# Kernel tuning notes

Hardware: AMD Instinct MI355X
Metric: run time of the kernel (lower is better)

The kernel has to match this reference:

```python
import jax, jax.numpy as jnp
import numpy as np

H = 2880      # hidden_size
I = 2880      # intermediate_size
E = 8         # num_experts
K = 4         # experts_per_token
N = 1024      # num tokens
EPS = 1e-5
ALPHA = 1.702
BETA = 1.0


def setup_inputs() -> dict:
    key = jax.random.key(0)
    ks = jax.random.split(key, 8)
    s = 0.02
    return {
        "x": jax.random.normal(ks[0], (N, H), jnp.float32),
        "norm_w": jnp.ones((H,), jnp.float32),
        "gate_w": jax.random.normal(ks[1], (E, H), jnp.float32) * s,
        "gate_b": jax.random.normal(ks[2], (E,), jnp.float32) * s,
        "w_gate_up": jax.random.normal(ks[3], (E, 2 * I, H), jnp.float32) * s,
        "b_gate_up": jax.random.normal(ks[4], (E, 2 * I), jnp.float32) * s,
        "w_down": jax.random.normal(ks[5], (E, H, I), jnp.float32) * s,
        "b_down": jax.random.normal(ks[6], (E, H), jnp.float32) * s,
    }


def reference(x, norm_w, gate_w, gate_b, w_gate_up, b_gate_up, w_down, b_down):
    # RMSNorm
    t = x * jax.lax.rsqrt(jnp.mean(x * x, axis=-1, keepdims=True) + EPS) * norm_w
    # Router gate (Linear with bias)
    logits = t @ gate_w.T + gate_b                      # [N, E]
    # Renormalize routing: top-k of logits, softmax over selected logits
    top_vals, top_idx = jax.lax.top_k(logits, K)        # [N, K]
    route_w = jax.nn.softmax(top_vals, axis=-1)         # [N, K]
    # Dense combine matrix [N, E] (zero for unselected experts)
    n_ar = jnp.arange(N)[:, None]
    R = jnp.zeros((N, E), t.dtype).at[n_ar, top_idx].add(route_w)
    # Fused gate_up projection per expert: [E, N, 2I]
    h = jnp.einsum('nh,eih->eni', t, w_gate_up) + b_gate_up[:, None, :]
    x_glu, x_lin = h[..., :I], h[..., I:]
    # SwiGLU with per-expert alpha/beta (all 1.702 / 1.0)
    act = x_glu * jax.nn.sigmoid(ALPHA * x_glu) * (x_lin + BETA)   # [E, N, I]
    # Down projection per expert: [E, N, H]
    outs = jnp.einsum('eni,ehi->enh', act, w_down) + b_down[:, None, :]
    # Weighted combine over selected experts + residual
    y = jnp.einsum('ne,enh->nh', R, outs)
    return x + y
```

## Files before the change

kernel.cpp:

```cpp
#include <hip/hip_runtime.h>
#include <hip/hip_bf16.h>

#define NTOK 1024
#define HDIM 2880
#define IDIM 2880
#define NEXP 8
#define BK 64
#define NT 45

typedef __attribute__((ext_vector_type(4))) float fx4;
typedef __attribute__((ext_vector_type(8))) short sx8;
typedef __attribute__((ext_vector_type(8))) unsigned short usx8;

typedef const __attribute__((address_space(1))) void* gas_p;
typedef __attribute__((address_space(3))) void* las_p;

__device__ __forceinline__ unsigned short f2bf(float f) {
  __hip_bfloat16 b = __float2bfloat16(f);
  return __builtin_bit_cast(unsigned short, b);
}
__device__ __forceinline__ usx8 cvt8(fx4 a, fx4 b) {
  usx8 u = {f2bf(a.x), f2bf(a.y), f2bf(a.z), f2bf(a.w),
            f2bf(b.x), f2bf(b.y), f2bf(b.z), f2bf(b.w)};
  return u;
}

#define MFMA16(a, b, c) __builtin_amdgcn_mfma_f32_16x16x32_bf16(a, b, c, 0, 0, 0)

__global__ __launch_bounds__(256) void init_out_k(const float* __restrict__ x,
                                                  float* __restrict__ out) {
  int i = blockIdx.x * 256 + threadIdx.x;
  ((fx4*)out)[i] = ((const fx4*)x)[i];
}

__global__ __launch_bounds__(256) void rms_router_k(
    const float* __restrict__ x, const float* __restrict__ norm_w,
    const float* __restrict__ gate_w, const float* __restrict__ gate_b,
    unsigned short* __restrict__ t_bf, int* __restrict__ cnt,
    int* __restrict__ tok, float* __restrict__ wgt) {
  const int n = blockIdx.x;
  const int tid = threadIdx.x;
  const int wid = tid >> 6, lane = tid & 63;
  const float* xr = x + (size_t)n * HDIM;

  float ss = 0.f;
  for (int h = tid; h < HDIM; h += 256) { float v = xr[h]; ss += v * v; }
  #pragma unroll
  for (int o = 32; o > 0; o >>= 1) ss += __shfl_down(ss, o);
  __shared__ float sred[4];
  if (lane == 0) sred[wid] = ss;
  __syncthreads();
  const float rstd =
      rsqrtf((sred[0] + sred[1] + sred[2] + sred[3]) * (1.0f / HDIM) + 1e-5f);

  float p[NEXP];
  #pragma unroll
  for (int e = 0; e < NEXP; e++) p[e] = 0.f;
  for (int h = tid; h < HDIM; h += 256) {
    float xv = xr[h] * norm_w[h];
    t_bf[(size_t)n * HDIM + h] = f2bf(xv * rstd);
    #pragma unroll
    for (int e = 0; e < NEXP; e++) p[e] += xv * gate_w[e * HDIM + h];
  }
  __shared__ float pls[4][NEXP];
  #pragma unroll
  for (int e = 0; e < NEXP; e++) {
    float v = p[e];
    #pragma unroll
    for (int o = 32; o > 0; o >>= 1) v += __shfl_down(v, o);
    if (lane == 0) pls[wid][e] = v;
  }
  __syncthreads();
  if (tid == 0) {
    float lg[NEXP];
    #pragma unroll
    for (int e = 0; e < NEXP; e++)
      lg[e] = (pls[0][e] + pls[1][e] + pls[2][e] + pls[3][e]) * rstd + gate_b[e];
    unsigned used = 0;
    float val[4];
    int idx[4];
    for (int k = 0; k < 4; k++) {
      float best = -1e30f;
      int bi = 0;
      for (int e = 0; e < NEXP; e++)
        if (!((used >> e) & 1u) && lg[e] > best) { best = lg[e]; bi = e; }
      used |= 1u << bi;
      val[k] = best;
      idx[k] = bi;
    }
    float sum = 0.f, w[4];
    for (int k = 0; k < 4; k++) { w[k] = expf(val[k] - val[0]); sum += w[k]; }
    for (int k = 0; k < 4; k++) {
      int e = idx[k];
      int slot = atomicAdd(&cnt[e], 1);
      tok[e * NTOK + slot] = n;
      wgt[e * NTOK + slot] = w[k] / sum;
    }
  }
}

__global__ __launch_bounds__(512, 4) void gemm1_k(
    const unsigned short* __restrict__ t_bf,
    const float* __restrict__ w_gate_up, const float* __restrict__ b_gate_up,
    const int* __restrict__ cnt, const int* __restrict__ tok,
    unsigned short* __restrict__ act_bf) {
  const int h = blockIdx.x;
  const int u = h >> 2, z = h & 3;
  const int e = u / 45;
  const int c0 = (u % 45) * 64;
  const int m0 = z * 256;
  const int ce = cnt[e];
  if (m0 >= ce) return;

  const int tid = threadIdx.x, lane = tid & 63, wid = tid >> 6;
  const int fr = lane & 15, fq = lane >> 4;
  const int wm = wid >> 1, wn = wid & 1;

  __shared__ __align__(16) unsigned short Ash[256 * 64];
  __shared__ __align__(16) unsigned short Bsh[128 * 64];

  const fx4 FZ = {0.f, 0.f, 0.f, 0.f};
  fx4 accG[4][2], accL[4][2];
  #pragma unroll
  for (int m = 0; m < 4; m++)
    #pragma unroll
    for (int n = 0; n < 2; n++) { accG[m][n] = FZ; accL[m][n] = FZ; }

  const unsigned short* gA[4];
  #pragma unroll
  for (int j = 0; j < 4; ++j) {
    int R = m0 + wid * 32 + j * 8 + (lane >> 3);
    int rc = R < ce ? R : ce - 1;
    gA[j] = t_bf + (size_t)tok[e * NTOK + rc] * HDIM +
            ((lane & 7) ^ ((lane >> 3) & 7)) * 8;
  }
  const int bR = tid >> 3, bC = tid & 7;
  const float* srcG = w_gate_up + (size_t)e * (2 * IDIM) * HDIM +
                      (size_t)(c0 + bR) * HDIM + bC * 8;
  const float* srcL = srcG + (size_t)IDIM * HDIM;
  const int bsw = (bC ^ (bR & 7)) * 8;

  fx4 rG0, rG1, rL0, rL1;
  rG0 = *(const fx4*)(srcG);
  rG1 = *(const fx4*)(srcG + 4);
  rL0 = *(const fx4*)(srcL);
  rL1 = *(const fx4*)(srcL + 4);

  for (int t = 0; t < NT; ++t) {
    const int ko = t * BK;
    __syncthreads();
    #pragma unroll
    for (int j = 0; j < 4; ++j)
      __builtin_amdgcn_global_load_lds((gas_p)(gA[j] + ko),
                                       (las_p)&Ash[(wid * 32 + j * 8) * 64], 16,
                                       0, 0);
    *(usx8*)&Bsh[bR * 64 + bsw] = cvt8(rG0, rG1);
    *(usx8*)&Bsh[(64 + bR) * 64 + bsw] = cvt8(rL0, rL1);
    __syncthreads();
    const int kf = (t + 1 < NT ? (t + 1) * BK : 0);
    rG0 = *(const fx4*)(srcG + kf);
    rG1 = *(const fx4*)(srcG + kf + 4);
    rL0 = *(const fx4*)(srcL + kf);
    rL1 = *(const fx4*)(srcL + kf + 4);
    #pragma unroll
    for (int ks = 0; ks < 2; ++ks) {
      const int rc = ks * 4 + fq;
      sx8 aF[4], bG[2], bL[2];
      #pragma unroll
      for (int m = 0; m < 4; ++m)
        aF[m] = *(const sx8*)&Ash[(wm * 64 + m * 16 + fr) * 64 +
                                  ((rc ^ (fr & 7)) * 8)];
      #pragma unroll
      for (int n = 0; n < 2; ++n) {
        bG[n] = *(const sx8*)&Bsh[(wn * 32 + n * 16 + fr) * 64 +
                                  ((rc ^ (fr & 7)) * 8)];
        bL[n] = *(const sx8*)&Bsh[(64 + wn * 32 + n * 16 + fr) * 64 +
                                  ((rc ^ (fr & 7)) * 8)];
      }
      __builtin_amdgcn_s_setprio(1);
      #pragma unroll
      for (int n = 0; n < 2; ++n)
        #pragma unroll
        for (int m = 0; m < 4; ++m) {
          accG[m][n] = MFMA16(aF[m], bG[n], accG[m][n]);
          accL[m][n] = MFMA16(aF[m], bL[n], accL[m][n]);
        }
      __builtin_amdgcn_s_setprio(0);
    }
  }

  #pragma unroll
  for (int n = 0; n < 2; ++n) {
    const int col = c0 + wn * 32 + n * 16 + fr;
    const float bg = b_gate_up[e * (2 * IDIM) + col];
    const float bl = b_gate_up[e * (2 * IDIM) + IDIM + col];
    #pragma unroll
    for (int m = 0; m < 4; ++m) {
      #pragma unroll
      for (int r = 0; r < 4; ++r) {
        int slot = m0 + wm * 64 + m * 16 + fq * 4 + r;
        if (slot < ce) {
          float g = accG[m][n][r] + bg;
          float l = accL[m][n][r] + bl;
          float a = g * (1.0f / (1.0f + __expf(-1.702f * g))) * (l + 1.0f);
          act_bf[((size_t)e * NTOK + slot) * IDIM + col] = f2bf(a);
        }
      }
    }
  }
}

__global__ __launch_bounds__(512, 4) void gemm2_k(
    const unsigned short* __restrict__ act_bf, const float* __restrict__ w_down,
    const float* __restrict__ b_down, const int* __restrict__ cnt,
    const int* __restrict__ tok, const float* __restrict__ wgt,
    float* __restrict__ out) {
  const int h = blockIdx.x;
  const int u = h >> 2, z = h & 3;
  const int e = u / 30;
  const int c0 = (u % 30) * 96;
  const int m0 = z * 256;
  const int ce = cnt[e];
  if (m0 >= ce) return;

  const int tid = threadIdx.x, lane = tid & 63, wid = tid >> 6;
  const int fr = lane & 15, fq = lane >> 4;
  const int wm = wid >> 1, wn = wid & 1;

  __shared__ __align__(16) unsigned short Ash[256 * 64];
  __shared__ __align__(16) unsigned short Bsh[96 * 64];

  const fx4 FZ = {0.f, 0.f, 0.f, 0.f};
  fx4 acc[4][3];
  #pragma unroll
  for (int m = 0; m < 4; m++)
    #pragma unroll
    for (int n = 0; n < 3; n++) acc[m][n] = FZ;

  const unsigned short* gA[4];
  #pragma unroll
  for (int j = 0; j < 4; ++j) {
    int R = m0 + wid * 32 + j * 8 + (lane >> 3);
    int rc = R < ce ? R : ce - 1;
    gA[j] = act_bf + ((size_t)e * NTOK + rc) * IDIM +
            ((lane & 7) ^ ((lane >> 3) & 7)) * 8;
  }
  const int bR0 = tid >> 3, bC0 = tid & 7;
  const float* wb = w_down + (size_t)e * HDIM * IDIM;
  const float* srcB0 = wb + (size_t)(c0 + bR0) * IDIM + bC0 * 8;
  const float* srcB1 = wb + (size_t)(c0 + 64 + bR0) * IDIM + bC0 * 8;
  const int bsw0 = (bC0 ^ (bR0 & 7)) * 8;

  fx4 r0a, r0b, r1a, r1b;
  r0a = *(const fx4*)(srcB0);
  r0b = *(const fx4*)(srcB0 + 4);
  if (tid < 256) {
    r1a = *(const fx4*)(srcB1);
    r1b = *(const fx4*)(srcB1 + 4);
  }

  for (int t = 0; t < NT; ++t) {
    const int ko = t * BK;
    __syncthreads();
    #pragma unroll
    for (int j = 0; j < 4; ++j)
      __builtin_amdgcn_global_load_lds((gas_p)(gA[j] + ko),
                                       (las_p)&Ash[(wid * 32 + j * 8) * 64], 16,
                                       0, 0);
    *(usx8*)&Bsh[bR0 * 64 + bsw0] = cvt8(r0a, r0b);
    if (tid < 256) *(usx8*)&Bsh[(64 + bR0) * 64 + bsw0] = cvt8(r1a, r1b);
    __syncthreads();
    const int kf = (t + 1 < NT ? (t + 1) * BK : 0);
    r0a = *(const fx4*)(srcB0 + kf);
    r0b = *(const fx4*)(srcB0 + kf + 4);
    if (tid < 256) {
      r1a = *(const fx4*)(srcB1 + kf);
      r1b = *(const fx4*)(srcB1 + kf + 4);
    }
    #pragma unroll
    for (int ks = 0; ks < 2; ++ks) {
      const int rc = ks * 4 + fq;
      sx8 aF[4], bB[3];
      #pragma unroll
      for (int m = 0; m < 4; ++m)
        aF[m] = *(const sx8*)&Ash[(wm * 64 + m * 16 + fr) * 64 +
                                  ((rc ^ (fr & 7)) * 8)];
      #pragma unroll
      for (int n = 0; n < 3; ++n)
        bB[n] = *(const sx8*)&Bsh[(wn * 48 + n * 16 + fr) * 64 +
                                  ((rc ^ (fr & 7)) * 8)];
      __builtin_amdgcn_s_setprio(1);
      #pragma unroll
      for (int n = 0; n < 3; ++n)
        #pragma unroll
        for (int m = 0; m < 4; ++m)
          acc[m][n] = MFMA16(aF[m], bB[n], acc[m][n]);
      __builtin_amdgcn_s_setprio(0);
    }
  }

  #pragma unroll
  for (int n = 0; n < 3; ++n) {
    const int col = c0 + wn * 48 + n * 16 + fr;
    const float bias = b_down[e * HDIM + col];
    #pragma unroll
    for (int m = 0; m < 4; ++m) {
      #pragma unroll
      for (int r = 0; r < 4; ++r) {
        int slot = m0 + wm * 64 + m * 16 + fq * 4 + r;
        if (slot < ce) {
          int token = tok[e * NTOK + slot];
          float w = wgt[e * NTOK + slot];
          atomicAdd(&out[(size_t)token * HDIM + col], w * (acc[m][n][r] + bias));
        }
      }
    }
  }
}

extern "C" void kernel_launch(void* const* d_in, const int* in_sizes, int n_in,
                              void* d_out, int out_size, void* d_ws,
                              size_t ws_size, hipStream_t stream) {
  const float* x = (const float*)d_in[0];
  const float* norm_w = (const float*)d_in[1];
  const float* gate_w = (const float*)d_in[2];
  const float* gate_b = (const float*)d_in[3];
  const float* w_gate_up = (const float*)d_in[4];
  const float* b_gate_up = (const float*)d_in[5];
  const float* w_down = (const float*)d_in[6];
  const float* b_down = (const float*)d_in[7];
  float* out = (float*)d_out;

  char* ws = (char*)d_ws;
  unsigned short* t_bf = (unsigned short*)ws;
  ws += (size_t)NTOK * HDIM * 2;
  unsigned short* act_bf = (unsigned short*)ws;
  ws += (size_t)NEXP * NTOK * IDIM * 2;
  int* cnt = (int*)ws;
  ws += 256;
  int* tok = (int*)ws;
  ws += (size_t)NEXP * NTOK * 4;
  float* wgt = (float*)ws;
  ws += (size_t)NEXP * NTOK * 4;

  hipMemsetAsync(cnt, 0, NEXP * sizeof(int), stream);
  init_out_k<<<2880, 256, 0, stream>>>(x, out);
  rms_router_k<<<NTOK, 256, 0, stream>>>(x, norm_w, gate_w, gate_b, t_bf, cnt,
                                         tok, wgt);
  gemm1_k<<<360 * 4, 512, 0, stream>>>(t_bf, w_gate_up, b_gate_up, cnt, tok,
                                       act_bf);
  gemm2_k<<<240 * 4, 512, 0, stream>>>(act_bf, w_down, b_down, cnt, tok, wgt,
                                       out);
}
```

Before: 654.3 us.

## Use 512-row M tiles with in-block M loop so each block streams weights once

Both expert GEMMs now launch one block per (expert, column tile) and loop over the M dimension in 512-row chunks, instead of splitting M into four 256-row blocks that each re-read and re-convert the fp32 weight tile. Each block reads its weight slice roughly once when the expert holds at most 512 tokens, which cuts redundant fp32 weight traffic and conversion. The cost is a smaller grid (360 and 240 blocks) with launch bounds lowered to one block per CU, twice the accumulator registers and a larger LDS A tile, which reduces occupancy and latency hiding. Experts with more than 512 tokens re-stream the weights in the loop.

```diff
diff --git a/kernel.cpp b/kernel.cpp
--- a/kernel.cpp
+++ b/kernel.cpp
@@ -99,219 +99,217 @@
   }
 }
 
-__global__ __launch_bounds__(512, 4) void gemm1_k(
+__global__ __launch_bounds__(512, 1) void gemm1_k(
     const unsigned short* __restrict__ t_bf,
     const float* __restrict__ w_gate_up, const float* __restrict__ b_gate_up,
     const int* __restrict__ cnt, const int* __restrict__ tok,
     unsigned short* __restrict__ act_bf) {
   const int h = blockIdx.x;
-  const int u = h >> 2, z = h & 3;
-  const int e = u / 45;
-  const int c0 = (u % 45) * 64;
-  const int m0 = z * 256;
+  const int e = h & 7;
+  const int c0 = (h >> 3) * 64;
   const int ce = cnt[e];
-  if (m0 >= ce) return;
 
   const int tid = threadIdx.x, lane = tid & 63, wid = tid >> 6;
   const int fr = lane & 15, fq = lane >> 4;
   const int wm = wid >> 1, wn = wid & 1;
-
-  __shared__ __align__(16) unsigned short Ash[256 * 64];
+  const int sw = ((lane & 7) ^ ((lane >> 3) & 7)) * 8;
+
+  __shared__ __align__(16) unsigned short Ash[512 * 64];
   __shared__ __align__(16) unsigned short Bsh[128 * 64];
 
-  const fx4 FZ = {0.f, 0.f, 0.f, 0.f};
-  fx4 accG[4][2], accL[4][2];
-  #pragma unroll
-  for (int m = 0; m < 4; m++)
-    #pragma unroll
-    for (int n = 0; n < 2; n++) { accG[m][n] = FZ; accL[m][n] = FZ; }
-
-  const unsigned short* gA[4];
-  #pragma unroll
-  for (int j = 0; j < 4; ++j) {
-    int R = m0 + wid * 32 + j * 8 + (lane >> 3);
-    int rc = R < ce ? R : ce - 1;
-    gA[j] = t_bf + (size_t)tok[e * NTOK + rc] * HDIM +
-            ((lane & 7) ^ ((lane >> 3) & 7)) * 8;
-  }
   const int bR = tid >> 3, bC = tid & 7;
-  const float* srcG = w_gate_up + (size_t)e * (2 * IDIM) * HDIM +
-                      (size_t)(c0 + bR) * HDIM + bC * 8;
-  const float* srcL = srcG + (size_t)IDIM * HDIM;
-  const int bsw = (bC ^ (bR & 7)) * 8;
-
-  fx4 rG0, rG1, rL0, rL1;
-  rG0 = *(const fx4*)(srcG);
-  rG1 = *(const fx4*)(srcG + 4);
-  rL0 = *(const fx4*)(srcL);
-  rL1 = *(const fx4*)(srcL + 4);
-
-  for (int t = 0; t < NT; ++t) {
-    const int ko = t * BK;
+  const float* wb = w_gate_up + (size_t)e * (2 * IDIM) * HDIM;
+  const float* srcG = wb + (size_t)(c0 + bR) * HDIM + bC * 8;
+  const float* srcL = wb + (size_t)(IDIM + c0 + bR) * HDIM + bC * 8;
+  const int bwG = bR * 64 + ((bC ^ (bR & 7)) * 8);
+  const int bwL = (64 + bR) * 64 + ((bC ^ ((64 + bR) & 7)) * 8);
+
+  for (int m0 = 0; m0 < ce; m0 += 512) {
+    const unsigned short* gA[8];
+    #pragma unroll
+    for (int j = 0; j < 8; ++j) {
+      int R = m0 + wid * 64 + j * 8 + (lane >> 3);
+      int rc = R < ce ? R : ce - 1;
+      gA[j] = t_bf + (size_t)tok[e * NTOK + rc] * HDIM + sw;
+    }
+    const fx4 FZ = {0.f, 0.f, 0.f, 0.f};
+    fx4 accG[8][2], accL[8][2];
+    #pragma unroll
+    for (int m = 0; m < 8; m++)
+      #pragma unroll
+      for (int n = 0; n < 2; n++) { accG[m][n] = FZ; accL[m][n] = FZ; }
+
+    fx4 rg0 = *(const fx4*)(srcG), rg1 = *(const fx4*)(srcG + 4);
+    fx4 rl0 = *(const fx4*)(srcL), rl1 = *(const fx4*)(srcL + 4);
+
+    for (int t = 0; t < NT; ++t) {
+      const int ko = t * BK;
+      __syncthreads();
+      #pragma unroll
+      for (int j = 0; j < 8; ++j)
+        __builtin_amdgcn_global_load_lds(
+            (gas_p)(gA[j] + ko), (las_p)&Ash[(wid * 64 + j * 8) * 64], 16, 0,
+            0);
+      *(usx8*)&Bsh[bwG] = cvt8(rg0, rg1);
+      *(usx8*)&Bsh[bwL] = cvt8(rl0, rl1);
+      __syncthreads();
+      if (t + 1 < NT) {
+        const int kf = (t + 1) * BK;
+        rg0 = *(const fx4*)(srcG + kf);
+        rg1 = *(const fx4*)(srcG + kf + 4);
+        rl0 = *(const fx4*)(srcL + kf);
+        rl1 = *(const fx4*)(srcL + kf + 4);
+      }
+      #pragma unroll
+      for (int ks = 0; ks < 2; ++ks) {
+        const int rk = ks * 4 + fq;
+        const int off = (rk ^ (fr & 7)) * 8;
+        sx8 aF[8], bG[2], bL[2];
+        #pragma unroll
+        for (int m = 0; m < 8; ++m)
+          aF[m] = *(const sx8*)&Ash[(wm * 128 + m * 16 + fr) * 64 + off];
+        #pragma unroll
+        for (int n = 0; n < 2; ++n) {
+          bG[n] = *(const sx8*)&Bsh[(wn * 32 + n * 16 + fr) * 64 + off];
+          bL[n] = *(const sx8*)&Bsh[(64 + wn * 32 + n * 16 + fr) * 64 + off];
+        }
+        __builtin_amdgcn_s_setprio(1);
+        #pragma unroll
+        for (int n = 0; n < 2; ++n)
+          #pragma unroll
+          for (int m = 0; m < 8; ++m) {
+            accG[m][n] = MFMA16(aF[m], bG[n], accG[m][n]);
+            accL[m][n] = MFMA16(aF[m], bL[n], accL[m][n]);
+          }
+        __builtin_amdgcn_s_setprio(0);
+      }
+    }
     __syncthreads();
-    #pragma unroll
-    for (int j = 0; j < 4; ++j)
-      __builtin_amdgcn_global_load_lds((gas_p)(gA[j] + ko),
-                                       (las_p)&Ash[(wid * 32 + j * 8) * 64], 16,
-                                       0, 0);
-    *(usx8*)&Bsh[bR * 64 + bsw] = cvt8(rG0, rG1);
-    *(usx8*)&Bsh[(64 + bR) * 64 + bsw] = cvt8(rL0, rL1);
-    __syncthreads();
-    const int kf = (t + 1 < NT ? (t + 1) * BK : 0);
-    rG0 = *(const fx4*)(srcG + kf);
-    rG1 = *(const fx4*)(srcG + kf + 4);
-    rL0 = *(const fx4*)(srcL + kf);
-    rL1 = *(const fx4*)(srcL + kf + 4);
-    #pragma unroll
-    for (int ks = 0; ks < 2; ++ks) {
-      const int rc = ks * 4 + fq;
-      sx8 aF[4], bG[2], bL[2];
-      #pragma unroll
-      for (int m = 0; m < 4; ++m)
-        aF[m] = *(const sx8*)&Ash[(wm * 64 + m * 16 + fr) * 64 +
-                                  ((rc ^ (fr & 7)) * 8)];
-      #pragma unroll
-      for (int n = 0; n < 2; ++n) {
-        bG[n] = *(const sx8*)&Bsh[(wn * 32 + n * 16 + fr) * 64 +
-                                  ((rc ^ (fr & 7)) * 8)];
-        bL[n] = *(const sx8*)&Bsh[(64 + wn * 32 + n * 16 + fr) * 64 +
-                                  ((rc ^ (fr & 7)) * 8)];
-      }
-      __builtin_amdgcn_s_setprio(1);
-      #pragma unroll
-      for (int n = 0; n < 2; ++n)
-        #pragma unroll
-        for (int m = 0; m < 4; ++m) {
-          accG[m][n] = MFMA16(aF[m], bG[n], accG[m][n]);
-          accL[m][n] = MFMA16(aF[m], bL[n], accL[m][n]);
+
+    #pragma unroll
+    for (int n = 0; n < 2; ++n) {
+      const int col = c0 + wn * 32 + n * 16 + fr;
+      const float bg = b_gate_up[e * (2 * IDIM) + col];
+      const float bl = b_gate_up[e * (2 * IDIM) + IDIM + col];
+      #pragma unroll
+      for (int m = 0; m < 8; ++m) {
+        #pragma unroll
+        for (int r = 0; r < 4; ++r) {
+          int slot = m0 + wm * 128 + m * 16 + fq * 4 + r;
+          if (slot < ce) {
+            float gv = accG[m][n][r] + bg;
+            float lv = accL[m][n][r] + bl;
+            float a = gv * (1.0f / (1.0f + __expf(-1.702f * gv))) * (lv + 1.0f);
+            act_bf[((size_t)e * NTOK + slot) * IDIM + col] = f2bf(a);
+          }
         }
-      __builtin_amdgcn_s_setprio(0);
-    }
-  }
-
-  #pragma unroll
-  for (int n = 0; n < 2; ++n) {
-    const int col = c0 + wn * 32 + n * 16 + fr;
-    const float bg = b_gate_up[e * (2 * IDIM) + col];
-    const float bl = b_gate_up[e * (2 * IDIM) + IDIM + col];
-    #pragma unroll
-    for (int m = 0; m < 4; ++m) {
-      #pragma unroll
-      for (int r = 0; r < 4; ++r) {
-        int slot = m0 + wm * 64 + m * 16 + fq * 4 + r;
-        if (slot < ce) {
-          float g = accG[m][n][r] + bg;
-          float l = accL[m][n][r] + bl;
-          float a = g * (1.0f / (1.0f + __expf(-1.702f * g))) * (l + 1.0f);
-          act_bf[((size_t)e * NTOK + slot) * IDIM + col] = f2bf(a);
-        }
-      }
-    }
-  }
-}
-
-__global__ __launch_bounds__(512, 4) void gemm2_k(
+      }
+    }
+  }
+}
+
+__global__ __launch_bounds__(512, 1) void gemm2_k(
     const unsigned short* __restrict__ act_bf, const float* __restrict__ w_down,
     const float* __restrict__ b_down, const int* __restrict__ cnt,
     const int* __restrict__ tok, const float* __restrict__ wgt,
     float* __restrict__ out) {
   const int h = blockIdx.x;
-  const int u = h >> 2, z = h & 3;
-  const int e = u / 30;
-  const int c0 = (u % 30) * 96;
-  const int m0 = z * 256;
+  const int e = h & 7;
+  const int c0 = (h >> 3) * 96;
   const int ce = cnt[e];
-  if (m0 >= ce) return;
 
   const int tid = threadIdx.x, lane = tid & 63, wid = tid >> 6;
   const int fr = lane & 15, fq = lane >> 4;
   const int wm = wid >> 1, wn = wid & 1;
-
-  __shared__ __align__(16) unsigned short Ash[256 * 64];
+  const int sw = ((lane & 7) ^ ((lane >> 3) & 7)) * 8;
+
+  __shared__ __align__(16) unsigned short Ash[512 * 64];
   __shared__ __align__(16) unsigned short Bsh[96 * 64];
 
-  const fx4 FZ = {0.f, 0.f, 0.f, 0.f};
-  fx4 acc[4][3];
-  #pragma unroll
-  for (int m = 0; m < 4; m++)
-    #pragma unroll
-    for (int n = 0; n < 3; n++) acc[m][n] = FZ;
-
-  const unsigned short* gA[4];
-  #pragma unroll
-  for (int j = 0; j < 4; ++j) {
-    int R = m0 + wid * 32 + j * 8 + (lane >> 3);
-    int rc = R < ce ? R : ce - 1;
-    gA[j] = act_bf + ((size_t)e * NTOK + rc) * IDIM +
-            ((lane & 7) ^ ((lane >> 3) & 7)) * 8;
-  }
   const int bR0 = tid >> 3, bC0 = tid & 7;
+  const int bR1 = (tid + 512) >> 3;
   const float* wb = w_down + (size_t)e * HDIM * IDIM;
   const float* srcB0 = wb + (size_t)(c0 + bR0) * IDIM + bC0 * 8;
-  const float* srcB1 = wb + (size_t)(c0 + 64 + bR0) * IDIM + bC0 * 8;
-  const int bsw0 = (bC0 ^ (bR0 & 7)) * 8;
-
-  fx4 r0a, r0b, r1a, r1b;
-  r0a = *(const fx4*)(srcB0);
-  r0b = *(const fx4*)(srcB0 + 4);
-  if (tid < 256) {
-    r1a = *(const fx4*)(srcB1);
-    r1b = *(const fx4*)(srcB1 + 4);
-  }
-
-  for (int t = 0; t < NT; ++t) {
-    const int ko = t * BK;
+  const float* srcB1 = wb + (size_t)(c0 + bR1) * IDIM + bC0 * 8;
+  const int bw0 = bR0 * 64 + ((bC0 ^ (bR0 & 7)) * 8);
+  const int bw1 = bR1 * 64 + ((bC0 ^ (bR1 & 7)) * 8);
+
+  for (int m0 = 0; m0 < ce; m0 += 512) {
+    const unsigned short* gA[8];
+    #pragma unroll
+    for (int j = 0; j < 8; ++j) {
+      int R = m0 + wid * 64 + j * 8 + (lane >> 3);
+      int rc = R < ce ? R : ce - 1;
+      gA[j] = act_bf + ((size_t)e * NTOK + rc) * IDIM + sw;
+    }
+    const fx4 FZ = {0.f, 0.f, 0.f, 0.f};
+    fx4 acc[8][3];
+    #pragma unroll
+    for (int m = 0; m < 8; m++)
+      #pragma unroll
+      for (int n = 0; n < 3; n++) acc[m][n] = FZ;
+
+    fx4 r0a = *(const fx4*)(srcB0), r0b = *(const fx4*)(srcB0 + 4);
+    fx4 r1a, r1b;
+    if (tid < 256) { r1a = *(const fx4*)(srcB1); r1b = *(const fx4*)(srcB1 + 4); }
+
+    for (int t = 0; t < NT; ++t) {
+      const int ko = t * BK;
+      __syncthreads();
+      #pragma unroll
+      for (int j = 0; j < 8; ++j)
+        __builtin_amdgcn_global_load_lds(
+            (gas_p)(gA[j] + ko), (las_p)&Ash[(wid * 64 + j * 8) * 64], 16, 0,
+            0);
+      *(usx8*)&Bsh[bw0] = cvt8(r0a, r0b);
+      if (tid < 256) *(usx8*)&Bsh[bw1] = cvt8(r1a, r1b);
+      __syncthreads();
+      if (t + 1 < NT) {
+        const int kf = (t + 1) * BK;
+        r0a = *(const fx4*)(srcB0 + kf);
+        r0b = *(const fx4*)(srcB0 + kf + 4);
+        if (tid < 256) {
+          r1a = *(const fx4*)(srcB1 + kf);
+          r1b = *(const fx4*)(srcB1 + kf + 4);
+        }
+      }
+      #pragma unroll
+      for (int ks = 0; ks < 2; ++ks) {
+        const int rk = ks * 4 + fq;
+        const int off = (rk ^ (fr & 7)) * 8;
+        sx8 aF[8], bB[3];
+        #pragma unroll
+        for (int m = 0; m < 8; ++m)
+          aF[m] = *(const sx8*)&Ash[(wm * 128 + m * 16 + fr) * 64 + off];
+        #pragma unroll
+        for (int n = 0; n < 3; ++n)
+          bB[n] = *(const sx8*)&Bsh[(wn * 48 + n * 16 + fr) * 64 + off];
+        __builtin_amdgcn_s_setprio(1);
+        #pragma unroll
+        for (int n = 0; n < 3; ++n)
+          #pragma unroll
+          for (int m = 0; m < 8; ++m)
+            acc[m][n] = MFMA16(aF[m], bB[n], acc[m][n]);
+        __builtin_amdgcn_s_setprio(0);
+      }
+    }
     __syncthreads();
-    #pragma unroll
-    for (int j = 0; j < 4; ++j)
-      __builtin_amdgcn_global_load_lds((gas_p)(gA[j] + ko),
-                                       (las_p)&Ash[(wid * 32 + j * 8) * 64], 16,
-                                       0, 0);
-    *(usx8*)&Bsh[bR0 * 64 + bsw0] = cvt8(r0a, r0b);
-    if (tid < 256) *(usx8*)&Bsh[(64 + bR0) * 64 + bsw0] = cvt8(r1a, r1b);
-    __syncthreads();
-    const int kf = (t + 1 < NT ? (t + 1) * BK : 0);
-    r0a = *(const fx4*)(srcB0 + kf);
-    r0b = *(const fx4*)(srcB0 + kf + 4);
-    if (tid < 256) {
-      r1a = *(const fx4*)(srcB1 + kf);
-      r1b = *(const fx4*)(srcB1 + kf + 4);
-    }
-    #pragma unroll
-    for (int ks = 0; ks < 2; ++ks) {
-      const int rc = ks * 4 + fq;
-      sx8 aF[4], bB[3];
-      #pragma unroll
-      for (int m = 0; m < 4; ++m)
-        aF[m] = *(const sx8*)&Ash[(wm * 64 + m * 16 + fr) * 64 +
-                                  ((rc ^ (fr & 7)) * 8)];
-      #pragma unroll
-      for (int n = 0; n < 3; ++n)
-        bB[n] = *(const sx8*)&Bsh[(wn * 48 + n * 16 + fr) * 64 +
-                                  ((rc ^ (fr & 7)) * 8)];
-      __builtin_amdgcn_s_setprio(1);
-      #pragma unroll
-      for (int n = 0; n < 3; ++n)
-        #pragma unroll
-        for (int m = 0; m < 4; ++m)
-          acc[m][n] = MFMA16(aF[m], bB[n], acc[m][n]);
-      __builtin_amdgcn_s_setprio(0);
-    }
-  }
-
-  #pragma unroll
-  for (int n = 0; n < 3; ++n) {
-    const int col = c0 + wn * 48 + n * 16 + fr;
-    const float bias = b_down[e * HDIM + col];
-    #pragma unroll
-    for (int m = 0; m < 4; ++m) {
-      #pragma unroll
-      for (int r = 0; r < 4; ++r) {
-        int slot = m0 + wm * 64 + m * 16 + fq * 4 + r;
-        if (slot < ce) {
-          int token = tok[e * NTOK + slot];
-          float w = wgt[e * NTOK + slot];
-          atomicAdd(&out[(size_t)token * HDIM + col], w * (acc[m][n][r] + bias));
+
+    #pragma unroll
+    for (int n = 0; n < 3; ++n) {
+      const int col = c0 + wn * 48 + n * 16 + fr;
+      const float bias = b_down[e * HDIM + col];
+      #pragma unroll
+      for (int m = 0; m < 8; ++m) {
+        #pragma unroll
+        for (int r = 0; r < 4; ++r) {
+          int slot = m0 + wm * 128 + m * 16 + fq * 4 + r;
+          if (slot < ce) {
+            int token = tok[e * NTOK + slot];
+            float w = wgt[e * NTOK + slot];
+            atomicAdd(&out[(size_t)token * HDIM + col],
+                      w * (acc[m][n][r] + bias));
+          }
         }
       }
     }
@@ -332,23 +330,23 @@
   float* out = (float*)d_out;
 
   char* ws = (char*)d_ws;
-  unsigned short* t_bf = (unsigned short*)ws;
-  ws += (size_t)NTOK * HDIM * 2;
-  unsigned short* act_bf = (unsigned short*)ws;
-  ws += (size_t)NEXP * NTOK * IDIM * 2;
-  int* cnt = (int*)ws;
-  ws += 256;
-  int* tok = (int*)ws;
-  ws += (size_t)NEXP * NTOK * 4;
-  float* wgt = (float*)ws;
-  ws += (size_t)NEXP * NTOK * 4;
+  size_t off = 0;
+  unsigned short* t_bf = (unsigned short*)(ws + off);
+  off += (size_t)NTOK * HDIM * 2;
+  unsigned short* act_bf = (unsigned short*)(ws + off);
+  off += (size_t)NEXP * NTOK * IDIM * 2;
+  int* cnt = (int*)(ws + off);
+  off += 256;
+  int* tok = (int*)(ws + off);
+  off += (size_t)NEXP * NTOK * 4;
+  float* wgt = (float*)(ws + off);
 
   hipMemsetAsync(cnt, 0, NEXP * sizeof(int), stream);
   init_out_k<<<2880, 256, 0, stream>>>(x, out);
   rms_router_k<<<NTOK, 256, 0, stream>>>(x, norm_w, gate_w, gate_b, t_bf, cnt,
                                          tok, wgt);
-  gemm1_k<<<360 * 4, 512, 0, stream>>>(t_bf, w_gate_up, b_gate_up, cnt, tok,
-                                       act_bf);
-  gemm2_k<<<240 * 4, 512, 0, stream>>>(act_bf, w_down, b_down, cnt, tok, wgt,
-                                       out);
-}
+  gemm1_k<<<45 * 8, 512, 0, stream>>>(t_bf, w_gate_up, b_gate_up, cnt, tok,
+                                      act_bf);
+  gemm2_k<<<30 * 8, 512, 0, stream>>>(act_bf, w_down, b_down, cnt, tok, wgt,
+                                      out);
+}
```

Measured after the change: 770.3 us. 1.18x slower.
